# Performance work log

Hardware: AMD Instinct MI355X
Metric: run time of the kernel (lower is better)

The kernel has to match this reference:

```python
import jax, jax.numpy as jnp
import numpy as np
from jax import lax

# cell-group layout (order matters): sr_esoma, sr_edend, sr_pv, sr_sst, sr_vip, pfc_esoma, pfc_edend, pfc_pv, pfc_sst, pfc_vip
SIZES = [512, 1024, 128, 128, 128, 512, 1024, 128, 128, 128]
OFF = np.cumsum([0] + SIZES)
(SR_ES, SR_ED, SR_PV, SR_SST, SR_VIP,
 PFC_ES, PFC_ED, PFC_PV, PFC_SST, PFC_VIP) = [slice(int(OFF[i]), int(OFF[i + 1])) for i in range(10)]
N = int(OFF[-1])            # 3840 total neurons
N_BR = 2                    # dendritic branches per excitatory soma
N_IN, N_OUT = 128, 3
T, B = 100, 32
DT, TAU = 10.0, 50.0
DECAY = DT / TAU            # hp['dt']/hp['tau']
NOISE_STD = 0.01            # hp['network_noise']

# mGluR slow-integration coefficients on PFC E-dendrites: alpha_me = dt / logspace(100..5000), tiled over branches
_tau_me = np.tile(np.logspace(np.log10(100.0), np.log10(5000.0), SIZES[6] // N_BR), N_BR)
ALPHA_ME = jnp.asarray(DT / _tau_me, dtype=jnp.float32)   # [1024]

_dend = np.zeros(N, dtype=bool)
_dend[SR_ED] = True
_dend[PFC_ED] = True
DEND_VEC = jnp.asarray(_dend)


def _build_mask():
    """Dale's-law connectivity mask: +1 excitatory rows, -1 inhibitory rows,
    dend->own-region soma blocked (handled by dend2soma), zero diagonal."""
    m = np.ones((N, N), dtype=np.float32)
    for inh in (SR_PV, SR_SST, SR_VIP, PFC_PV, PFC_SST, PFC_VIP):
        m[inh, :] = -1.0
    m[SR_ED, SR_ES] = 0.0
    m[PFC_ED, PFC_ES] = 0.0
    np.fill_diagonal(m, 0.0)
    return m


def setup_inputs() -> dict:
    key = jax.random.key(0)
    ks = jax.random.split(key, 5)
    return {
        "x": jax.random.normal(ks[0], (T, B, N_IN), jnp.float32),
        "noise": jax.random.normal(ks[1], (T, B, N), jnp.float32),
        "w_rec": jax.random.normal(ks[2], (N, N), jnp.float32) / np.float32(np.sqrt(N)),
        "w_in": jax.random.normal(ks[3], (N_IN, N), jnp.float32) / np.float32(np.sqrt(N_IN)),
        "b": jnp.zeros((N,), jnp.float32),
        "d2s": jnp.ones((SIZES[1] + SIZES[6],), jnp.float32),
        "w_out": jax.random.normal(ks[4], (SIZES[0], N_OUT), jnp.float32) / np.float32(np.sqrt(SIZES[0])),
        "b_out": jnp.zeros((N_OUT,), jnp.float32),
        "mask": jnp.asarray(_build_mask()),
    }


def reference(x, noise, w_rec, w_in, b, d2s, w_out, b_out, mask):
    # effective recurrent weights: magnitude from w_rec, sign/sparsity from mask
    w_eff = jnp.abs(w_rec) * mask
    d2s_sr = d2s[:SIZES[1]].reshape(N_BR, SIZES[0])
    d2s_pfc = d2s[SIZES[1]:].reshape(N_BR, SIZES[5])
    nb = x.shape[1]
    h0 = jnp.zeros((nb, N), x.dtype)
    ime0 = jnp.zeros((nb, SIZES[6]), x.dtype)
    noise_scale = jnp.sqrt(jnp.asarray(2.0 * DECAY, x.dtype)) * NOISE_STD

    def step(carry, inp):
        h, ime = carry
        x_t, n_t = inp
        # rates: ReLU for somas/interneurons, sigmoidal dendritic nonlinearity for dendrites
        r = jnp.where(DEND_VEC[None, :], jax.nn.sigmoid(h), jax.nn.relu(h))
        pre = r @ w_eff + x_t @ w_in + b                      # [B, N]
        # dendrite -> soma coupling, summed over branches
        pre = pre.at[:, SR_ES].add(
            jnp.einsum('bkn,kn->bn', r[:, SR_ED].reshape(nb, N_BR, SIZES[0]), d2s_sr))
        pre = pre.at[:, PFC_ES].add(
            jnp.einsum('bkn,kn->bn', r[:, PFC_ED].reshape(nb, N_BR, SIZES[5]), d2s_pfc))
        # mGluR slow integration on PFC E-dendrites (per-dendrite time constants)
        ime_new = (1.0 - ALPHA_ME) * ime + ALPHA_ME * jax.nn.relu(pre[:, PFC_ED])
        pre = pre.at[:, PFC_ED].add(ime_new)
        # leaky integration with injected noise
        h_new = (1.0 - DECAY) * h + DECAY * pre + noise_scale * n_t
        out_t = r[:, SR_ES] @ w_out + b_out                   # readout from SR E somas
        return (h_new, ime_new), out_t

    _, outs = lax.scan(step, (h0, ime0), (x, noise))
    return outs   # [T, B, N_OUT]
```

## Files before the change

### kernel.cpp

```cpp
#include <hip/hip_runtime.h>
#include <math.h>

typedef _Float16 f16;
typedef f16 f16x8 __attribute__((ext_vector_type(8)));
typedef float f32x4 __attribute__((ext_vector_type(4)));

#define NTOT 3840
#define KP   3968
#define BATCH 32
#define TSTEPS 100
#define NIN 128
#define NWG 241
#define RSTRIDE (BATCH*KP)
#define BROW 7952

__device__ __forceinline__ bool is_dend(int k){
  return (k>=512 && k<1536) || (k>=2432 && k<3456);
}
__device__ __forceinline__ bool is_inh(int k){
  return (k>=1536 && k<1920) || (k>=3456 && k<3840);
}
__device__ __forceinline__ ushort f2h(float v){ f16 h=(f16)v; return *(ushort*)&h; }
__device__ __forceinline__ float h2f(ushort u){ f16 h=*(f16*)&u; return (float)h; }

__global__ __launch_bounds__(256) void k_prep_w(const float* __restrict__ w_rec,
    const float* __restrict__ w_in, ushort* __restrict__ WT){
  __shared__ ushort tile[64][72];
  const int bid = blockIdx.x;
  const int kt = bid / 60, nt = bid % 60;
  const int k0 = kt*64, n0 = nt*64;
  const int t = threadIdx.x;
  const int tr = t>>2, tq = t&3;
  const int k = k0 + tr;
  const int cbase = n0 + tq*16;
  if (k < NTOT){
    const float sgn = is_inh(k) ? -1.f : 1.f;
    const bool rowSr  = (k>=512  && k<1536);
    const bool rowPfc = (k>=2432 && k<3456);
    #pragma unroll
    for (int q=0;q<4;q++){
      float4 w = *(const float4*)(w_rec + (size_t)k*NTOT + cbase + q*4);
      float v[4] = {sgn*fabsf(w.x), sgn*fabsf(w.y), sgn*fabsf(w.z), sgn*fabsf(w.w)};
      #pragma unroll
      for (int e=0;e<4;e++){
        const int n = cbase + q*4 + e;
        if (n==k || (rowSr && n<512) || (rowPfc && n>=1920 && n<2432)) v[e]=0.f;
        tile[tr][tq*16+q*4+e] = f2h(v[e]);
      }
    }
  } else {
    const float* src = w_in + (size_t)(k-NTOT)*NTOT + cbase;
    #pragma unroll
    for (int q=0;q<4;q++){
      float4 w = *(const float4*)(src + q*4);
      tile[tr][tq*16+q*4+0] = f2h(w.x);
      tile[tr][tq*16+q*4+1] = f2h(w.y);
      tile[tr][tq*16+q*4+2] = f2h(w.z);
      tile[tr][tq*16+q*4+3] = f2h(w.w);
    }
  }
  __syncthreads();
  const int n  = n0 + tr;
  const int kq = tq*16;
  uint u[8];
  #pragma unroll
  for (int q=0;q<8;q++)
    u[q] = (uint)tile[kq+2*q][tr] | ((uint)tile[kq+2*q+1][tr] << 16);
  uint4* dst = (uint4*)(WT + (size_t)n*KP + k0 + kq);
  dst[0] = make_uint4(u[0],u[1],u[2],u[3]);
  dst[1] = make_uint4(u[4],u[5],u[6],u[7]);
}

__global__ void k_init(const float* __restrict__ x, ushort* __restrict__ r0,
                       unsigned* __restrict__ bar){
  int i = blockIdx.x*blockDim.x + threadIdx.x;
  int nthr = gridDim.x*blockDim.x;
  for (int e=i; e<1024; e+=nthr) bar[e] = 0u;
  for (int e=i; e<BATCH*KP; e+=nthr){
    int b = e / KP, k = e % KP;
    float v = (k<NTOT) ? (is_dend(k)?0.5f:0.f) : x[b*NIN + (k-NTOT)];
    r0[e] = f2h(v);
  }
}

__global__ __launch_bounds__(512,1) void k_run(
    const ushort* __restrict__ WTu, ushort* rbase,
    const float* __restrict__ noise, const float* __restrict__ x,
    const float* __restrict__ bvec, const float* __restrict__ d2s,
    const float* __restrict__ w_out, const float* __restrict__ b_out,
    float* __restrict__ out, unsigned* bar)
{
  __shared__ ushort Blds[16*BROW/2];
  __shared__ f32x4 red[3][2][64];
  __shared__ float pre_lds[32][16];
  const f16* WT = (const f16*)WTu;
  const int bid = blockIdx.x;
  const int tid = threadIdx.x;
  const int wv = tid>>6, l = tid&63, l15 = l&15, lh = l>>4;
  const int bh = wv&1, kw = wv>>1;
  const int n0 = bid*16;
  const int ub = tid>>4, uc = tid&15;
  const int n  = n0 + uc;
  const float NS = 0.0063245553203367585f;

  float hr=0.f, im=0.f, bv=0.f, dA=0.f, dB=0.f, al=0.f;
  bool cSR=false, cPFC=false, cME=false, dendF=false;
  if (bid < 240){
    bv = bvec[n];
    cSR  = (n0 < 512);
    cPFC = (n0 >= 1920 && n0 < 2432);
    cME  = (n0 >= 2432 && n0 < 3456);
    dendF = (n0>=512 && n0<1536) || cME;
    if (cSR){  dA=d2s[n];       dB=d2s[512+n]; }
    if (cPFC){ const int j=n-1920; dA=d2s[1024+j]; dB=d2s[1536+j]; }
    if (cME){
      const float LN10 = 2.302585092994046f;
      const float CEXP = 1.6989700043360187f/511.0f;
      const int j = n-2432;
      al = expf(-LN10*(1.0f + CEXP*(float)(j&511)));
    }
    for (int c = tid; c < 16*496; c += 512){
      const int row = c / 496;
      const int kc  = c - row*496;
      f16x8 v = *(const f16x8*)(WT + (size_t)(n0+row)*KP + kc*8);
      *(f16x8*)((char*)Blds + row*BROW + kc*16) = v;
    }
  }

  float wo[3][8];
  float bo0=0.f, bo1=0.f, bo2=0.f;
  if (bid == 240){
    #pragma unroll
    for (int o=0;o<3;o++)
      #pragma unroll
      for (int i=0;i<8;i++) wo[o][i] = w_out[(l*8+i)*3 + o];
    bo0 = b_out[0]; bo1 = b_out[1]; bo2 = b_out[2];
  }
  __syncthreads();

  const int xg = bid & 7;
  const unsigned mycnt = (xg==0) ? 31u : 30u;
  unsigned* xcnt = bar + xg*32;
  unsigned* xep  = bar + 256 + xg*32;
  unsigned* gcnt = bar + 512;
  unsigned* gep  = bar + 544;

  const char* bbase = (const char*)Blds + l15*BROW + kw*1984 + lh*16;

  for (int t=0; t<TSTEPS; t++){
    const ushort* rcu = rbase + (size_t)t*RSTRIDE;
    ushort*       rnu = rbase + (size_t)(t+1)*RSTRIDE;
    const f16* rc = (const f16*)rcu;

    if (bid < 240){
      const float nz_pf = noise[(size_t)t*BATCH*NTOT + ub*NTOT + n];
      float cA = 0.f, cB = 0.f;
      if (cSR){
        cA = h2f(rcu[ub*KP + 512 +n]); cB = h2f(rcu[ub*KP + 1024+n]);
      } else if (cPFC){
        const int j = n-1920;
        cA = h2f(rcu[ub*KP + 2432+j]); cB = h2f(rcu[ub*KP + 2944+j]);
      }

      f32x4 acc; acc.x=0.f; acc.y=0.f; acc.z=0.f; acc.w=0.f;
      {
        const f16* pa = rc + (size_t)(bh*16+l15)*KP + kw*992 + lh*8;
        #pragma unroll
        for (int ks=0; ks<31; ks++){
          f16x8 a = *(const f16x8*)(pa + ks*32);
          f16x8 b = *(const f16x8*)(bbase + ks*64);
          acc = __builtin_amdgcn_mfma_f32_16x16x32_f16(a, b, acc, 0,0,0);
        }
      }
      if (kw > 0) red[kw-1][bh][l] = acc;
      __syncthreads();
      if (kw == 0){
        #pragma unroll
        for (int w=0;w<3;w++) acc += red[w][bh][l];
        #pragma unroll
        for (int rg=0;rg<4;rg++)
          pre_lds[bh*16 + lh*4 + rg][l15] = acc[rg];
      }
      __syncthreads();

      {
        float p = pre_lds[ub][uc] + bv;
        p += cA*dA + cB*dB;
        if (cME){
          im = (1.f-al)*im + al*fmaxf(p,0.f); p += im;
        }
        hr = 0.8f*hr + 0.2f*p + NS*nz_pf;
        const float rv = dendF ? (1.f/(1.f+expf(-hr))) : fmaxf(hr,0.f);
        __hip_atomic_store(&rnu[ub*KP + n], f2h(rv),
                           __ATOMIC_RELAXED, __HIP_MEMORY_SCOPE_AGENT);
      }
    } else {
      #pragma unroll
      for (int q=0;q<12;q++){
        const int p = wv*12 + q;
        const int b = p/3, o = p%3;
        f16x8 rv8 = *(const f16x8*)(rc + (size_t)b*KP + l*8);
        float s = 0.f;
        #pragma unroll
        for (int i=0;i<8;i++) s += (float)rv8[i] * wo[o][i];
        #pragma unroll
        for (int off=32; off; off>>=1) s += __shfl_down(s, off);
        if (l==0){
          const float bo = (o==0)?bo0:((o==1)?bo1:bo2);
          out[t*BATCH*3 + b*3 + o] = s + bo;
        }
      }
      if (t+1 < TSTEPS && tid < 256){
        const int b = tid>>3, j = (tid&7)*16;
        const float* xs = x + (size_t)(t+1)*BATCH*NIN + b*NIN + j;
        #pragma unroll
        for (int q=0;q<4;q++){
          float4 v = *(const float4*)(xs + q*4);
          uint u0 = (uint)f2h(v.x) | ((uint)f2h(v.y)<<16);
          uint u1 = (uint)f2h(v.z) | ((uint)f2h(v.w)<<16);
          uint* dst = (uint*)&rnu[b*KP + NTOT + j + q*4];
          __hip_atomic_store(dst,   u0, __ATOMIC_RELAXED, __HIP_MEMORY_SCOPE_AGENT);
          __hip_atomic_store(dst+1, u1, __ATOMIC_RELAXED, __HIP_MEMORY_SCOPE_AGENT);
        }
      }
    }

    if (t+1 < TSTEPS){
      __syncthreads();
      if (tid == 0){
        unsigned old = __hip_atomic_fetch_add(xcnt, 1u,
                          __ATOMIC_RELAXED, __HIP_MEMORY_SCOPE_AGENT);
        if (old == mycnt*(unsigned)(t+1) - 1u){
          unsigned g = __hip_atomic_fetch_add(gcnt, 1u,
                          __ATOMIC_RELAXED, __HIP_MEMORY_SCOPE_AGENT);
          if (g == 8u*(unsigned)(t+1) - 1u){
            __hip_atomic_store(gep, (unsigned)(t+1),
                          __ATOMIC_RELAXED, __HIP_MEMORY_SCOPE_AGENT);
          } else {
            while (__hip_atomic_load(gep, __ATOMIC_RELAXED,
                          __HIP_MEMORY_SCOPE_AGENT) < (unsigned)(t+1))
              __builtin_amdgcn_s_sleep(2);
          }
          __hip_atomic_store(xep, (unsigned)(t+1),
                          __ATOMIC_RELAXED, __HIP_MEMORY_SCOPE_AGENT);
        } else {
          while (__hip_atomic_load(xep, __ATOMIC_RELAXED,
                          __HIP_MEMORY_SCOPE_AGENT) < (unsigned)(t+1))
            __builtin_amdgcn_s_sleep(2);
        }
        asm volatile("" ::: "memory");
      }
      __syncthreads();
    }
  }
}

extern "C" void kernel_launch(void* const* d_in, const int* in_sizes, int n_in,
                              void* d_out, int out_size, void* d_ws, size_t ws_size,
                              hipStream_t stream) {
  const float* x     = (const float*)d_in[0];
  const float* noise = (const float*)d_in[1];
  const float* w_rec = (const float*)d_in[2];
  const float* w_in  = (const float*)d_in[3];
  const float* bvec  = (const float*)d_in[4];
  const float* d2s   = (const float*)d_in[5];
  const float* w_out = (const float*)d_in[6];
  const float* b_out = (const float*)d_in[7];
  float* out = (float*)d_out;

  char* ws = (char*)d_ws;
  ushort*   WT    = (ushort*)(ws);
  ushort*   rbase = (ushort*)(ws + 30474240);
  unsigned* bar   = (unsigned*)(ws + 56123392);

  k_prep_w<<<3720,256,0,stream>>>(w_rec, w_in, WT);
  k_init<<<64,256,0,stream>>>(x, rbase, bar);
  k_run<<<NWG,512,0,stream>>>(WT, rbase, noise, x, bvec, d2s,
                              w_out, b_out, out, bar);
}
```

Before: 1.001 ms.

## Double workgroup size to split K over eight waves and flatten barrier wait

Each workgroup now runs 1024 threads, so the K reduction per column tile is split across 8 wave-pairs (four of 512 K, four of 480 K) instead of 4, which halves each wave's serial MFMA chain and adds a larger LDS reduction. Non-leader workgroups in the grid barrier now spin directly on the global epoch flag instead of a per-group flag, with a shorter sleep. The readout and epilogue paths are restricted to the first 512 threads or 3 waves. This trades fewer registers per thread and more reduction traffic, plus more global spinners on one cache line, for shorter per-step critical latency.

```diff
diff --git a/kernel.cpp b/kernel.cpp
--- a/kernel.cpp
+++ b/kernel.cpp
@@ -83,7 +83,7 @@
   }
 }
 
-__global__ __launch_bounds__(512,1) void k_run(
+__global__ __launch_bounds__(1024,1) void k_run(
     const ushort* __restrict__ WTu, ushort* rbase,
     const float* __restrict__ noise, const float* __restrict__ x,
     const float* __restrict__ bvec, const float* __restrict__ d2s,
@@ -91,13 +91,15 @@
     float* __restrict__ out, unsigned* bar)
 {
   __shared__ ushort Blds[16*BROW/2];
-  __shared__ f32x4 red[3][2][64];
+  __shared__ f32x4 red[7][2][64];
   __shared__ float pre_lds[32][16];
   const f16* WT = (const f16*)WTu;
   const int bid = blockIdx.x;
   const int tid = threadIdx.x;
   const int wv = tid>>6, l = tid&63, l15 = l&15, lh = l>>4;
   const int bh = wv&1, kw = wv>>1;
+  const int kbase = (kw<4) ? (kw<<9) : (2048 + (kw-4)*480);
+  const int nst   = (kw<4) ? 16 : 15;
   const int n0 = bid*16;
   const int ub = tid>>4, uc = tid&15;
   const int n  = n0 + uc;
@@ -106,20 +108,22 @@
   float hr=0.f, im=0.f, bv=0.f, dA=0.f, dB=0.f, al=0.f;
   bool cSR=false, cPFC=false, cME=false, dendF=false;
   if (bid < 240){
-    bv = bvec[n];
-    cSR  = (n0 < 512);
-    cPFC = (n0 >= 1920 && n0 < 2432);
-    cME  = (n0 >= 2432 && n0 < 3456);
-    dendF = (n0>=512 && n0<1536) || cME;
-    if (cSR){  dA=d2s[n];       dB=d2s[512+n]; }
-    if (cPFC){ const int j=n-1920; dA=d2s[1024+j]; dB=d2s[1536+j]; }
-    if (cME){
-      const float LN10 = 2.302585092994046f;
-      const float CEXP = 1.6989700043360187f/511.0f;
-      const int j = n-2432;
-      al = expf(-LN10*(1.0f + CEXP*(float)(j&511)));
-    }
-    for (int c = tid; c < 16*496; c += 512){
+    if (tid < 512){
+      bv = bvec[n];
+      cSR  = (n0 < 512);
+      cPFC = (n0 >= 1920 && n0 < 2432);
+      cME  = (n0 >= 2432 && n0 < 3456);
+      dendF = (n0>=512 && n0<1536) || cME;
+      if (cSR){  dA=d2s[n];       dB=d2s[512+n]; }
+      if (cPFC){ const int j=n-1920; dA=d2s[1024+j]; dB=d2s[1536+j]; }
+      if (cME){
+        const float LN10 = 2.302585092994046f;
+        const float CEXP = 1.6989700043360187f/511.0f;
+        const int j = n-2432;
+        al = expf(-LN10*(1.0f + CEXP*(float)(j&511)));
+      }
+    }
+    for (int c = tid; c < 16*496; c += 1024){
       const int row = c / 496;
       const int kc  = c - row*496;
       f16x8 v = *(const f16x8*)(WT + (size_t)(n0+row)*KP + kc*8);
@@ -141,11 +145,10 @@
   const int xg = bid & 7;
   const unsigned mycnt = (xg==0) ? 31u : 30u;
   unsigned* xcnt = bar + xg*32;
-  unsigned* xep  = bar + 256 + xg*32;
   unsigned* gcnt = bar + 512;
   unsigned* gep  = bar + 544;
 
-  const char* bbase = (const char*)Blds + l15*BROW + kw*1984 + lh*16;
+  const char* bb = (const char*)Blds + l15*BROW + kbase*2 + lh*16;
 
   for (int t=0; t<TSTEPS; t++){
     const ushort* rcu = rbase + (size_t)t*RSTRIDE;
@@ -153,22 +156,24 @@
     const f16* rc = (const f16*)rcu;
 
     if (bid < 240){
-      const float nz_pf = noise[(size_t)t*BATCH*NTOT + ub*NTOT + n];
-      float cA = 0.f, cB = 0.f;
-      if (cSR){
-        cA = h2f(rcu[ub*KP + 512 +n]); cB = h2f(rcu[ub*KP + 1024+n]);
-      } else if (cPFC){
-        const int j = n-1920;
-        cA = h2f(rcu[ub*KP + 2432+j]); cB = h2f(rcu[ub*KP + 2944+j]);
+      float nz_pf = 0.f, cA = 0.f, cB = 0.f;
+      if (tid < 512){
+        nz_pf = noise[(size_t)t*BATCH*NTOT + ub*NTOT + n];
+        if (cSR){
+          cA = h2f(rcu[ub*KP + 512 +n]); cB = h2f(rcu[ub*KP + 1024+n]);
+        } else if (cPFC){
+          const int j = n-1920;
+          cA = h2f(rcu[ub*KP + 2432+j]); cB = h2f(rcu[ub*KP + 2944+j]);
+        }
       }
 
       f32x4 acc; acc.x=0.f; acc.y=0.f; acc.z=0.f; acc.w=0.f;
       {
-        const f16* pa = rc + (size_t)(bh*16+l15)*KP + kw*992 + lh*8;
-        #pragma unroll
-        for (int ks=0; ks<31; ks++){
+        const f16* pa = rc + (size_t)(bh*16+l15)*KP + kbase + lh*8;
+        #pragma unroll 4
+        for (int ks=0; ks<nst; ks++){
           f16x8 a = *(const f16x8*)(pa + ks*32);
-          f16x8 b = *(const f16x8*)(bbase + ks*64);
+          f16x8 b = *(const f16x8*)(bb + ks*64);
           acc = __builtin_amdgcn_mfma_f32_16x16x32_f16(a, b, acc, 0,0,0);
         }
       }
@@ -176,14 +181,14 @@
       __syncthreads();
       if (kw == 0){
         #pragma unroll
-        for (int w=0;w<3;w++) acc += red[w][bh][l];
+        for (int w=0;w<7;w++) acc += red[w][bh][l];
         #pragma unroll
         for (int rg=0;rg<4;rg++)
           pre_lds[bh*16 + lh*4 + rg][l15] = acc[rg];
       }
       __syncthreads();
 
-      {
+      if (tid < 512){
         float p = pre_lds[ub][uc] + bv;
         p += cA*dA + cB*dB;
         if (cME){
@@ -195,19 +200,23 @@
                            __ATOMIC_RELAXED, __HIP_MEMORY_SCOPE_AGENT);
       }
     } else {
-      #pragma unroll
-      for (int q=0;q<12;q++){
-        const int p = wv*12 + q;
-        const int b = p/3, o = p%3;
-        f16x8 rv8 = *(const f16x8*)(rc + (size_t)b*KP + l*8);
-        float s = 0.f;
-        #pragma unroll
-        for (int i=0;i<8;i++) s += (float)rv8[i] * wo[o][i];
-        #pragma unroll
-        for (int off=32; off; off>>=1) s += __shfl_down(s, off);
-        if (l==0){
-          const float bo = (o==0)?bo0:((o==1)?bo1:bo2);
-          out[t*BATCH*3 + b*3 + o] = s + bo;
+      if (wv < 3){
+        #pragma unroll
+        for (int q=0;q<32;q++){
+          const int p = wv*32 + q;
+          if (p < 96){
+            const int b = p/3, o = p%3;
+            f16x8 rv8 = *(const f16x8*)(rc + (size_t)b*KP + l*8);
+            float s = 0.f;
+            #pragma unroll
+            for (int i=0;i<8;i++) s += (float)rv8[i] * wo[o][i];
+            #pragma unroll
+            for (int off=32; off; off>>=1) s += __shfl_down(s, off);
+            if (l==0){
+              const float bo = (o==0)?bo0:((o==1)?bo1:bo2);
+              out[t*BATCH*3 + b*3 + o] = s + bo;
+            }
+          }
         }
       }
       if (t+1 < TSTEPS && tid < 256){
@@ -233,21 +242,13 @@
         if (old == mycnt*(unsigned)(t+1) - 1u){
           unsigned g = __hip_atomic_fetch_add(gcnt, 1u,
                           __ATOMIC_RELAXED, __HIP_MEMORY_SCOPE_AGENT);
-          if (g == 8u*(unsigned)(t+1) - 1u){
+          if (g == 8u*(unsigned)(t+1) - 1u)
             __hip_atomic_store(gep, (unsigned)(t+1),
                           __ATOMIC_RELAXED, __HIP_MEMORY_SCOPE_AGENT);
-          } else {
-            while (__hip_atomic_load(gep, __ATOMIC_RELAXED,
-                          __HIP_MEMORY_SCOPE_AGENT) < (unsigned)(t+1))
-              __builtin_amdgcn_s_sleep(2);
-          }
-          __hip_atomic_store(xep, (unsigned)(t+1),
-                          __ATOMIC_RELAXED, __HIP_MEMORY_SCOPE_AGENT);
-        } else {
-          while (__hip_atomic_load(xep, __ATOMIC_RELAXED,
-                          __HIP_MEMORY_SCOPE_AGENT) < (unsigned)(t+1))
-            __builtin_amdgcn_s_sleep(2);
-        }
+        }
+        while (__hip_atomic_load(gep, __ATOMIC_RELAXED,
+                      __HIP_MEMORY_SCOPE_AGENT) < (unsigned)(t+1))
+          __builtin_amdgcn_s_sleep(1);
         asm volatile("" ::: "memory");
       }
       __syncthreads();
@@ -275,6 +276,6 @@
 
   k_prep_w<<<3720,256,0,stream>>>(w_rec, w_in, WT);
   k_init<<<64,256,0,stream>>>(x, rbase, bar);
-  k_run<<<NWG,512,0,stream>>>(WT, rbase, noise, x, bvec, d2s,
-                              w_out, b_out, out, bar);
-}
+  k_run<<<NWG,1024,0,stream>>>(WT, rbase, noise, x, bvec, d2s,
+                               w_out, b_out, out, bar);
+}
```

Result: slower. 3.919 ms (+291.6%).
